# Kernel tuning notes

Measured on AMD Instinct MI355X. Metric: run time of the kernel, lower is better.

Reference implementation:

```python
import jax, jax.numpy as jnp
import numpy as np

P, F_IN, HG, C, T, E, HOUT = 4096, 64, 64, 64, 32, 65536, 12
LEAKY_SLOPE = 0.2
LN_EPS = 1e-5


def setup_inputs() -> dict:
    key = jax.random.key(0)
    ks = jax.random.split(key, 14)
    g = lambda k, shape, scale: (jax.random.normal(k, shape, jnp.float32) * scale)
    return {
        "X": jax.random.normal(ks[0], (1, P, F_IN, T), jnp.float32),
        "edge_index": jax.random.randint(ks[1], (T, 2, E), 0, P, jnp.int32),
        # GATv2 params (single head)
        "Wl": g(ks[2], (F_IN, HG), 0.1),
        "Wr": g(ks[3], (F_IN, HG), 0.1),
        "att": g(ks[4], (HG,), 0.1),
        "gat_b": g(ks[5], (HG,), 0.02),
        # 1x1 time conv (HG -> C) and 1x1 residual conv (F_IN -> C)
        "W_time": g(ks[6], (C, HG), 0.1),
        "b_time": g(ks[7], (C,), 0.02),
        "W_res": g(ks[8], (C, F_IN), 0.1),
        "b_res": g(ks[9], (C,), 0.02),
        # LayerNorm over channel dim C
        "ln_g": jnp.ones((C,), jnp.float32),
        "ln_b": jnp.zeros((C,), jnp.float32),
        # final conv: Conv2d(in=T, out=HOUT, kernel=(1, C)) -> weight (HOUT, T, C)
        "W_final": g(ks[10], (HOUT, T, C), 0.05),
        "b_final": g(ks[11], (HOUT,), 0.02),
    }


def reference(X, edge_index, Wl, Wr, att, gat_b, W_time, b_time, W_res, b_res,
              ln_g, ln_b, W_final, b_final):
    Pn = X.shape[1]

    def gat_t(x, edges):
        # x: (P, F_IN), edges: (2, E) with edges[0]=src j, edges[1]=dst i
        src, dst = edges[0], edges[1]
        hl = x @ Wl                      # (P, HG) messages
        hr = x @ Wr                      # (P, HG) query side
        e = jax.nn.leaky_relu(hl[src] + hr[dst], LEAKY_SLOPE) @ att  # (E,)
        emax = jax.ops.segment_max(e, dst, num_segments=Pn)
        ex = jnp.exp(e - emax[dst])
        den = jax.ops.segment_sum(ex, dst, num_segments=Pn)
        alpha = ex / den[dst]            # softmax over in-edges of each dst
        return jax.ops.segment_sum(alpha[:, None] * hl[src], dst,
                                   num_segments=Pn) + gat_b  # (P, HG)

    xs = jnp.moveaxis(X[0], -1, 0)                     # (T, P, F_IN)
    X_hat = jax.nn.relu(jax.vmap(gat_t)(xs, edge_index))  # (T, P, HG)

    th = jnp.einsum('tph,ch->tpc', X_hat, W_time) + b_time  # time conv 1x1
    rs = jnp.einsum('tpf,cf->tpc', xs, W_res) + b_res       # residual conv 1x1
    y = jax.nn.relu(th + rs)                                 # (T, P, C)

    mu = jnp.mean(y, axis=-1, keepdims=True)
    var = jnp.var(y, axis=-1, keepdims=True)
    yn = (y - mu) * jax.lax.rsqrt(var + LN_EPS) * ln_g + ln_b  # (T, P, C)

    # final conv: in-channels = T, kernel (1, C) -> contract over t and c
    out = jnp.einsum('tpc,otc->po', yn, W_final) + b_final     # (P, HOUT)
    return out[None]                                           # (1, P, HOUT)
```

## Files before the change

### kernel.cpp

```cpp
#include <hip/hip_runtime.h>
#include <math.h>

#define NP 4096
#define F_IN 64
#define HG 64
#define NC 64
#define NT 32
#define NE 65536
#define HOUT 12
#define LEAKY 0.2f
#define LN_EPS 1e-5f

template <int CTRL>
__device__ __forceinline__ float dppadd(float v, float x) {
    int r = __builtin_amdgcn_update_dpp(0, __builtin_bit_cast(int, x), CTRL, 0xF, 0xF, false);
    return v + __builtin_bit_cast(float, r);
}
__device__ __forceinline__ float rowsum16(float v) {
    v = dppadd<0x128>(v, v);
    v = dppadd<0x124>(v, v);
    v = dppadd<0x122>(v, v);
    v = dppadd<0x121>(v, v);
    return v;
}
__device__ __forceinline__ float xrowsum(float v) {
    v = dppadd<0x142>(v, v);
    v = dppadd<0x143>(v, v);
    return v;
}
__device__ __forceinline__ float rdlane(float v, int l) {
    return __builtin_bit_cast(float, __builtin_amdgcn_readlane(__builtin_bit_cast(int, v), l));
}
__device__ __forceinline__ float wavered63(float v) {
    v = rowsum16(v);
    v = xrowsum(v);
    return rdlane(v, 63);
}
__device__ __forceinline__ float laneXorSum(float v) {
    v += __shfl_xor(v, 16, 64);
    v += __shfl_xor(v, 32, 64);
    return v;
}
__device__ __forceinline__ int waveSumInt(int v) {
#pragma unroll
    for (int d = 1; d < 64; d <<= 1) v += __shfl_xor(v, d, 64);
    return v;
}

#define FMA4(Acomp, B, r)                                                     \
    acc[r][0] += (Acomp) * (B).x; acc[r][1] += (Acomp) * (B).y;               \
    acc[r][2] += (Acomp) * (B).z; acc[r][3] += (Acomp) * (B).w;

__global__ __launch_bounds__(256) void k_prep(const float* __restrict__ W_time,
        const float* __restrict__ W_res,
        float* __restrict__ wtT, float* __restrict__ wrT) {
    int b = blockIdx.x, tid = threadIdx.x;
    if (b < 16) {
        int i = b * 256 + tid;
        wtT[i] = W_time[(i & 63) * 64 + (i >> 6)];
    } else {
        int i = (b - 16) * 256 + tid;
        wrT[i] = W_res[(i & 63) * 64 + (i >> 6)];
    }
}

__global__ __launch_bounds__(256) void k_hlhr(const float* __restrict__ X,
        const float* __restrict__ Wl, const float* __restrict__ Wr,
        const float* __restrict__ wrT, const float* __restrict__ b_res,
        float* __restrict__ hl, float* __restrict__ hr, float* __restrict__ rs) {
    __shared__ float xs[2][F_IN][36];
    __shared__ float bk[F_IN][132];
    int p0 = blockIdx.x * 2, tid = threadIdx.x;
    const float4* Xp = (const float4*)(X + (size_t)p0 * F_IN * NT);
    for (int i4 = tid; i4 < 1024; i4 += 256) {
        int pp = i4 >> 9, f = (i4 >> 3) & 63, t0 = (i4 & 7) * 4;
        *(float4*)&xs[pp][f][t0] = Xp[i4];
    }
    for (int i = tid; i < F_IN * HG; i += 256) {
        int f = i >> 6, h = i & 63;
        bk[f][h] = Wl[i];
        bk[f][64 + h] = Wr[i];
    }
    __syncthreads();
    {
        int ng = tid & 31, tg = tid >> 5;
        int n0 = ng * 4, col = (ng & 15) * 4, t0 = tg * 4;
        float acc[8][4];
#pragma unroll
        for (int i = 0; i < 8; ++i)
#pragma unroll
            for (int j = 0; j < 4; ++j) acc[i][j] = 0.f;
#pragma unroll 4
        for (int f = 0; f < F_IN; ++f) {
            float4 B = *(const float4*)&bk[f][n0];
            float4 A0 = *(const float4*)&xs[0][f][t0];
            float4 A1 = *(const float4*)&xs[1][f][t0];
            FMA4(A0.x, B, 0) FMA4(A0.y, B, 1) FMA4(A0.z, B, 2) FMA4(A0.w, B, 3)
            FMA4(A1.x, B, 4) FMA4(A1.y, B, 5) FMA4(A1.z, B, 6) FMA4(A1.w, B, 7)
        }
#pragma unroll
        for (int pp = 0; pp < 2; ++pp) {
#pragma unroll
            for (int i = 0; i < 4; ++i) {
                size_t rb = ((size_t)(t0 + i) * NP + p0 + pp) * HG;
                float4 v;
                v.x = acc[pp * 4 + i][0]; v.y = acc[pp * 4 + i][1];
                v.z = acc[pp * 4 + i][2]; v.w = acc[pp * 4 + i][3];
                if (ng < 16) *(float4*)&hl[rb + col] = v;
                else         *(float4*)&hr[rb + col] = v;
            }
        }
    }
    __syncthreads();
    for (int i = tid; i < F_IN * NC; i += 256) bk[i >> 6][i & 63] = wrT[i];
    __syncthreads();
    {
        int cg = tid & 15, tg = tid >> 4;
        int c0 = cg * 4, t0 = tg * 2;
        float4 br4 = *(const float4*)&b_res[c0];
        float acc[4][4];
#pragma unroll
        for (int i = 0; i < 4; ++i) {
            acc[i][0] = br4.x; acc[i][1] = br4.y; acc[i][2] = br4.z; acc[i][3] = br4.w;
        }
#pragma unroll 4
        for (int f = 0; f < F_IN; ++f) {
            float4 B = *(const float4*)&bk[f][c0];
            float2 A0 = *(const float2*)&xs[0][f][t0];
            float2 A1 = *(const float2*)&xs[1][f][t0];
            FMA4(A0.x, B, 0) FMA4(A0.y, B, 1)
            FMA4(A1.x, B, 2) FMA4(A1.y, B, 3)
        }
#pragma unroll
        for (int pp = 0; pp < 2; ++pp) {
#pragma unroll
            for (int i = 0; i < 2; ++i) {
                float4 v;
                v.x = acc[pp * 2 + i][0]; v.y = acc[pp * 2 + i][1];
                v.z = acc[pp * 2 + i][2]; v.w = acc[pp * 2 + i][3];
                *(float4*)&rs[((size_t)(t0 + i) * NP + p0 + pp) * NC + c0] = v;
            }
        }
    }
}

__global__ __launch_bounds__(256) void k_count(const int* __restrict__ EI,
        int* __restrict__ cnt2, int* __restrict__ segsum2) {
    __shared__ int loc[1024];
    int b = blockIdx.x;
    int j = b >> 3;
    int t = (b & 7) + 8 * (j & 3);
    int cr = j >> 2;
    int c = cr & 3, r = cr >> 2;
    int tid = threadIdx.x;
    loc[tid] = 0; loc[tid + 256] = 0; loc[tid + 512] = 0; loc[tid + 768] = 0;
    __syncthreads();
    int base = r << 10;
    const int4* dstA = (const int4*)(EI + (size_t)t * 2 * NE + NE) + c * (NE / 16);
    for (int i = tid; i < NE / 16; i += 256) {
        int4 d = dstA[i];
        if ((d.x >> 10) == r) atomicAdd(&loc[d.x - base], 1);
        if ((d.y >> 10) == r) atomicAdd(&loc[d.y - base], 1);
        if ((d.z >> 10) == r) atomicAdd(&loc[d.z - base], 1);
        if ((d.w >> 10) == r) atomicAdd(&loc[d.w - base], 1);
    }
    __syncthreads();
    int o = (t * 4 + c) * NP + base + tid;
    cnt2[o] = loc[tid];
    cnt2[o + 256] = loc[tid + 256];
    cnt2[o + 512] = loc[tid + 512];
    cnt2[o + 768] = loc[tid + 768];
    int wv = tid >> 6, lane = tid & 63;
    int s = loc[wv * 256 + lane] + loc[wv * 256 + lane + 64]
          + loc[wv * 256 + lane + 128] + loc[wv * 256 + lane + 192];
    s = waveSumInt(s);
    if (lane == 0) segsum2[(t * 4 + c) * 16 + r * 4 + wv] = s;
}

__global__ __launch_bounds__(256) void k_scan(const int* __restrict__ cnt2,
        const int* __restrict__ segsum2, int* __restrict__ cnt,
        int* __restrict__ start, int* __restrict__ start2) {
    __shared__ int sc[256];
    __shared__ int preS;
    int b = blockIdx.x;
    int t = b >> 4, seg = b & 15;
    int tid = threadIdx.x;
    if (tid < 64) {
        int c = tid >> 4, s = tid & 15;
        int v = (s < seg) ? segsum2[(t * 4 + c) * 16 + s] : 0;
        v = waveSumInt(v);
        if (tid == 0) preS = v;
    }
    int d = seg * 256 + tid;
    int q0 = cnt2[(t * 4 + 0) * NP + d];
    int q1 = cnt2[(t * 4 + 1) * NP + d];
    int q2 = cnt2[(t * 4 + 2) * NP + d];
    int q3 = cnt2[(t * 4 + 3) * NP + d];
    int deg = q0 + q1 + q2 + q3;
    sc[tid] = deg;
    __syncthreads();
    int pre = preS;
    for (int dd = 1; dd < 256; dd <<= 1) {
        int v = (tid >= dd) ? sc[tid - dd] : 0;
        __syncthreads();
        sc[tid] += v;
        __syncthreads();
    }
    int exc = sc[tid] - deg;
    int st = t * NE + pre + exc;
    cnt[t * NP + d] = deg;
    start[t * NP + d] = st;
    start2[(t * 4 + 0) * NP + d] = st; st += q0;
    start2[(t * 4 + 1) * NP + d] = st; st += q1;
    start2[(t * 4 + 2) * NP + d] = st; st += q2;
    start2[(t * 4 + 3) * NP + d] = st;
}

__global__ __launch_bounds__(256) void k_fill(const int* __restrict__ EI,
        const int* __restrict__ start2, int* __restrict__ ssrc) {
    __shared__ int curs_l[1024];
    int b = blockIdx.x;
    int j = b >> 3;
    int t = (b & 7) + 8 * (j & 3);
    int cr = j >> 2;
    int c = cr & 3, r = cr >> 2;
    int tid = threadIdx.x;
    int base = r << 10;
    int o = (t * 4 + c) * NP + base + tid;
    curs_l[tid] = start2[o];
    curs_l[tid + 256] = start2[o + 256];
    curs_l[tid + 512] = start2[o + 512];
    curs_l[tid + 768] = start2[o + 768];
    __syncthreads();
    const int4* srcA = (const int4*)(EI + (size_t)t * 2 * NE) + c * (NE / 16);
    const int4* dstA = (const int4*)(EI + (size_t)t * 2 * NE + NE) + c * (NE / 16);
    for (int i = tid; i < NE / 16; i += 256) {
        int4 s = srcA[i];
        int4 d = dstA[i];
        if ((d.x >> 10) == r) { int sl = atomicAdd(&curs_l[d.x - base], 1); ssrc[sl] = s.x; }
        if ((d.y >> 10) == r) { int sl = atomicAdd(&curs_l[d.y - base], 1); ssrc[sl] = s.y; }
        if ((d.z >> 10) == r) { int sl = atomicAdd(&curs_l[d.z - base], 1); ssrc[sl] = s.z; }
        if ((d.w >> 10) == r) { int sl = atomicAdd(&curs_l[d.w - base], 1); ssrc[sl] = s.w; }
    }
}

__global__ __launch_bounds__(256) void k_gat(const float* __restrict__ hl,
        float* __restrict__ hr,
        const int* __restrict__ start, const int* __restrict__ cnt,
        const int* __restrict__ ssrc,
        const float* __restrict__ att, const float* __restrict__ gat_b) {
    __shared__ int sidx[4][64];
    int b = blockIdx.x;
    int k = b >> 3;
    int t = (b & 7) + 8 * (k >> 10);
    int ws = threadIdx.x >> 6;
    int i = (k & 1023) * 4 + ws;
    int lane = threadIdx.x & 63;
    int row = lane >> 4;
    int c0 = (lane & 15) * 4;
    size_t nbase = ((size_t)t * NP + i) * HG;
    const float* hlt = hl + (size_t)t * NP * HG;
    float4 r4 = *(const float4*)&hr[nbase + c0];
    float4 at4 = *(const float4*)&att[c0];
    int s0 = start[t * NP + i];
    int deg = cnt[t * NP + i];
    float l = 0.f;
    float4 acc = {0.f, 0.f, 0.f, 0.f};
    for (int base = 0; base < deg; base += 64) {
        int chunk = deg - base;
        chunk = (chunk < 64) ? chunk : 64;
        int stage = (lane < chunk) ? lane : 0;
        sidx[ws][lane] = ssrc[s0 + base + stage];
        int nfull = chunk & ~7;
        int j = 0;
        for (; j < nfull; j += 8) {
            int src0 = sidx[ws][j + row];
            int src1 = sidx[ws][j + 4 + row];
            float4 h0 = *(const float4*)&hlt[((size_t)src0 << 6) + c0];
            float4 h1 = *(const float4*)&hlt[((size_t)src1 << 6) + c0];
            float4 z0, z1;
            z0.x = h0.x + r4.x; z0.y = h0.y + r4.y; z0.z = h0.z + r4.z; z0.w = h0.w + r4.w;
            z1.x = h1.x + r4.x; z1.y = h1.y + r4.y; z1.z = h1.z + r4.z; z1.w = h1.w + r4.w;
            z0.x = fmaxf(z0.x, LEAKY * z0.x); z0.y = fmaxf(z0.y, LEAKY * z0.y);
            z0.z = fmaxf(z0.z, LEAKY * z0.z); z0.w = fmaxf(z0.w, LEAKY * z0.w);
            z1.x = fmaxf(z1.x, LEAKY * z1.x); z1.y = fmaxf(z1.y, LEAKY * z1.y);
            z1.z = fmaxf(z1.z, LEAKY * z1.z); z1.w = fmaxf(z1.w, LEAKY * z1.w);
            float e0 = rowsum16(z0.x * at4.x + z0.y * at4.y + z0.z * at4.z + z0.w * at4.w);
            float e1 = rowsum16(z1.x * at4.x + z1.y * at4.y + z1.z * at4.z + z1.w * at4.w);
            float w0 = __expf(e0);
            float w1 = __expf(e1);
            l += w0 + w1;
            acc.x += w0 * h0.x + w1 * h1.x;
            acc.y += w0 * h0.y + w1 * h1.y;
            acc.z += w0 * h0.z + w1 * h1.z;
            acc.w += w0 * h0.w + w1 * h1.w;
        }
        for (; j < chunk; j += 4) {
            int jj = j + row;
            int src = sidx[ws][(jj < chunk) ? jj : 0];
            float4 ha = *(const float4*)&hlt[((size_t)src << 6) + c0];
            float4 za;
            za.x = ha.x + r4.x; za.y = ha.y + r4.y; za.z = ha.z + r4.z; za.w = ha.w + r4.w;
            za.x = fmaxf(za.x, LEAKY * za.x);
            za.y = fmaxf(za.y, LEAKY * za.y);
            za.z = fmaxf(za.z, LEAKY * za.z);
            za.w = fmaxf(za.w, LEAKY * za.w);
            float ep = za.x * at4.x + za.y * at4.y + za.z * at4.z + za.w * at4.w;
            float e = rowsum16(ep);
            float w = __expf(e);
            w = (jj < chunk) ? w : 0.f;
            l += w;
            acc.x += w * ha.x; acc.y += w * ha.y; acc.z += w * ha.z; acc.w += w * ha.w;
        }
    }
    float lt = laneXorSum(l);
    acc.x = laneXorSum(acc.x);
    acc.y = laneXorSum(acc.y);
    acc.z = laneXorSum(acc.z);
    acc.w = laneXorSum(acc.w);
    if (row == 0) {
        float inv = (deg > 0) ? (1.0f / lt) : 0.f;
        float4 gb = *(const float4*)&gat_b[c0];
        float4 o;
        o.x = fmaxf(acc.x * inv + gb.x, 0.f);
        o.y = fmaxf(acc.y * inv + gb.y, 0.f);
        o.z = fmaxf(acc.z * inv + gb.z, 0.f);
        o.w = fmaxf(acc.w * inv + gb.w, 0.f);
        *(float4*)&hr[nbase + c0] = o;
    }
}

__global__ __launch_bounds__(256) void k_post(const float* __restrict__ Xhat,
        const float* __restrict__ wtT, const float* __restrict__ b_time,
        const float* __restrict__ rs, const float* __restrict__ ln_g,
        const float* __restrict__ ln_b, float* __restrict__ yn) {
    __shared__ float in_t[64][68];
    __shared__ float bk[64][68];
    int bx = blockIdx.x;
    int j = bx >> 3;
    int t = (bx & 7) + 8 * (j & 3);
    int p0 = (j >> 2) * 64;
    int tid = threadIdx.x;
    const float4* src = (const float4*)(Xhat + ((size_t)t * NP + p0) * HG);
    for (int i4 = tid; i4 < 1024; i4 += 256) {
        int pp = i4 >> 4, c4 = (i4 & 15) * 4;
        *(float4*)&in_t[pp][c4] = src[i4];
    }
    const float4* wsrc = (const float4*)wtT;
    for (int i4 = tid; i4 < 1024; i4 += 256) {
        int h = i4 >> 4, c4 = (i4 & 15) * 4;
        *(float4*)&bk[h][c4] = wsrc[i4];
    }
    __syncthreads();
    int cg = tid & 15, pg = tid >> 4;
    int c0 = cg * 4, pl = pg * 4;
    float4 bt4 = *(const float4*)&b_time[c0];
    float acc[4][4];
#pragma unroll
    for (int i = 0; i < 4; ++i) {
        acc[i][0] = bt4.x; acc[i][1] = bt4.y; acc[i][2] = bt4.z; acc[i][3] = bt4.w;
    }
#pragma unroll
    for (int k4 = 0; k4 < 16; ++k4) {
        float4 A0 = *(const float4*)&in_t[pl + 0][k4 * 4];
        float4 A1 = *(const float4*)&in_t[pl + 1][k4 * 4];
        float4 A2 = *(const float4*)&in_t[pl + 2][k4 * 4];
        float4 A3 = *(const float4*)&in_t[pl + 3][k4 * 4];
        float4 B0 = *(const float4*)&bk[k4 * 4 + 0][c0];
        FMA4(A0.x, B0, 0) FMA4(A1.x, B0, 1) FMA4(A2.x, B0, 2) FMA4(A3.x, B0, 3)
        float4 B1 = *(const float4*)&bk[k4 * 4 + 1][c0];
        FMA4(A0.y, B1, 0) FMA4(A1.y, B1, 1) FMA4(A2.y, B1, 2) FMA4(A3.y, B1, 3)
        float4 B2 = *(const float4*)&bk[k4 * 4 + 2][c0];
        FMA4(A0.z, B2, 0) FMA4(A1.z, B2, 1) FMA4(A2.z, B2, 2) FMA4(A3.z, B2, 3)
        float4 B3 = *(const float4*)&bk[k4 * 4 + 3][c0];
        FMA4(A0.w, B3, 0) FMA4(A1.w, B3, 1) FMA4(A2.w, B3, 2) FMA4(A3.w, B3, 3)
    }
    float4 lg = *(const float4*)&ln_g[c0];
    float4 lb = *(const float4*)&ln_b[c0];
#pragma unroll
    for (int i = 0; i < 4; ++i) {
        size_t prow = (size_t)t * NP + p0 + pl + i;
        float4 r4 = *(const float4*)&rs[prow * NC + c0];
        float y0 = fmaxf(acc[i][0] + r4.x, 0.f), y1 = fmaxf(acc[i][1] + r4.y, 0.f);
        float y2 = fmaxf(acc[i][2] + r4.z, 0.f), y3 = fmaxf(acc[i][3] + r4.w, 0.f);
        float s = rowsum16(y0 + y1 + y2 + y3);
        float ss = rowsum16(y0 * y0 + y1 * y1 + y2 * y2 + y3 * y3);
        float mu = s * (1.f / 64.f);
        float var = ss * (1.f / 64.f) - mu * mu;
        float rsd = rsqrtf(var + LN_EPS);
        float4 o;
        o.x = (y0 - mu) * rsd * lg.x + lb.x;
        o.y = (y1 - mu) * rsd * lg.y + lb.y;
        o.z = (y2 - mu) * rsd * lg.z + lb.z;
        o.w = (y3 - mu) * rsd * lg.w + lb.w;
        *(float4*)&yn[prow * NC + c0] = o;
    }
}

__global__ __launch_bounds__(256) void k_final(const float* __restrict__ yn,
        const float* __restrict__ Wf, const float* __restrict__ bf,
        float* __restrict__ out) {
    int p = blockIdx.x * 4 + (threadIdx.x >> 6);
    int lane = threadIdx.x & 63;
    float acc[HOUT];
#pragma unroll
    for (int o = 0; o < HOUT; ++o) acc[o] = 0.f;
    for (int k = 0; k < NT; ++k) {
        float yv = yn[((size_t)k * NP + p) * NC + lane];
#pragma unroll
        for (int o = 0; o < HOUT; ++o)
            acc[o] += yv * Wf[(size_t)o * NT * NC + k * NC + lane];
    }
#pragma unroll
    for (int o = 0; o < HOUT; ++o) {
        float s = wavered63(acc[o]);
        if (lane == 0) out[p * HOUT + o] = s + bf[o];
    }
}

extern "C" void kernel_launch(void* const* d_in, const int* in_sizes, int n_in,
                              void* d_out, int out_size, void* d_ws, size_t ws_size,
                              hipStream_t stream) {
    const float* X      = (const float*)d_in[0];
    const int*   EI     = (const int*)d_in[1];
    const float* Wl     = (const float*)d_in[2];
    const float* Wr     = (const float*)d_in[3];
    const float* att    = (const float*)d_in[4];
    const float* gat_b  = (const float*)d_in[5];
    const float* W_time = (const float*)d_in[6];
    const float* b_time = (const float*)d_in[7];
    const float* W_res  = (const float*)d_in[8];
    const float* b_res  = (const float*)d_in[9];
    const float* ln_g   = (const float*)d_in[10];
    const float* ln_b   = (const float*)d_in[11];
    const float* Wf     = (const float*)d_in[12];
    const float* bf     = (const float*)d_in[13];
    float* out = (float*)d_out;

    char* ws = (char*)d_ws;
    const size_t MB = 1024 * 1024;
    float* hl    = (float*)(ws);
    float* hr    = (float*)(ws + 32 * MB);
    float* rs    = (float*)(ws + 64 * MB);
    int*   ssrc  = (int*)  (ws + 96 * MB);
    int*   cnt   = (int*)  (ws + 104 * MB);
    int*   strt  = (int*)  (ws + 104 * MB + 512 * 1024);
    float* wtT   = (float*)(ws + 105 * MB);
    float* wrT   = (float*)(ws + 105 * MB + 16384);
    int*   segs2 = (int*)  (ws + 105 * MB + 32768);
    int*   cnt2  = (int*)  (ws + 106 * MB);
    int*   strt2 = (int*)  (ws + 108 * MB);
    float* yn    = hl;

    k_prep <<<32, 256, 0, stream>>>(W_time, W_res, wtT, wrT);
    k_hlhr <<<NP / 2, 256, 0, stream>>>(X, Wl, Wr, wrT, b_res, hl, hr, rs);
    k_count<<<512, 256, 0, stream>>>(EI, cnt2, segs2);
    k_scan <<<NT * 16, 256, 0, stream>>>(cnt2, segs2, cnt, strt, strt2);
    k_fill <<<512, 256, 0, stream>>>(EI, strt2, ssrc);
    k_gat  <<<(NT * NP) / 4, 256, 0, stream>>>(hl, hr, strt, cnt, ssrc, att, gat_b);
    k_post <<<NT * (NP / 64), 256, 0, stream>>>(hr, wtT, b_time, rs, ln_g, ln_b, yn);
    k_final<<<NP / 4, 256, 0, stream>>>(yn, Wf, bf, out);
}
```

Before: 284.0 us.

## Fuse post-processing with final conv and accumulate output via atomics

Merges the time conv, residual add, LayerNorm, and final T×C contraction into one kernel. Each block handles 64 nodes over 4 time steps, accumulates partial outputs in registers, and atomically adds them into an output that k_prep pre-fills with the bias. This removes the write and re-read of the full yn intermediate (T·P·C floats) and one launch. The cost is fewer blocks (512), serialized time steps per block and atomic contention on the output. It also vectorizes weight loads into shared memory in k_hlhr.

```diff
diff --git a/kernel.cpp b/kernel.cpp
--- a/kernel.cpp
+++ b/kernel.cpp
@@ -23,19 +23,6 @@
     v = dppadd<0x121>(v, v);
     return v;
 }
-__device__ __forceinline__ float xrowsum(float v) {
-    v = dppadd<0x142>(v, v);
-    v = dppadd<0x143>(v, v);
-    return v;
-}
-__device__ __forceinline__ float rdlane(float v, int l) {
-    return __builtin_bit_cast(float, __builtin_amdgcn_readlane(__builtin_bit_cast(int, v), l));
-}
-__device__ __forceinline__ float wavered63(float v) {
-    v = rowsum16(v);
-    v = xrowsum(v);
-    return rdlane(v, 63);
-}
 __device__ __forceinline__ float laneXorSum(float v) {
     v += __shfl_xor(v, 16, 64);
     v += __shfl_xor(v, 32, 64);
@@ -52,15 +39,18 @@
     acc[r][2] += (Acomp) * (B).z; acc[r][3] += (Acomp) * (B).w;
 
 __global__ __launch_bounds__(256) void k_prep(const float* __restrict__ W_time,
-        const float* __restrict__ W_res,
-        float* __restrict__ wtT, float* __restrict__ wrT) {
+        const float* __restrict__ W_res, const float* __restrict__ bf,
+        float* __restrict__ wtT, float* __restrict__ wrT, float* __restrict__ out) {
     int b = blockIdx.x, tid = threadIdx.x;
     if (b < 16) {
         int i = b * 256 + tid;
         wtT[i] = W_time[(i & 63) * 64 + (i >> 6)];
-    } else {
+    } else if (b < 32) {
         int i = (b - 16) * 256 + tid;
         wrT[i] = W_res[(i & 63) * 64 + (i >> 6)];
+    } else {
+        int i = (b - 32) * 256 + tid;
+        out[i] = bf[i % HOUT];
     }
 }
 
@@ -76,10 +66,12 @@
         int pp = i4 >> 9, f = (i4 >> 3) & 63, t0 = (i4 & 7) * 4;
         *(float4*)&xs[pp][f][t0] = Xp[i4];
     }
-    for (int i = tid; i < F_IN * HG; i += 256) {
-        int f = i >> 6, h = i & 63;
-        bk[f][h] = Wl[i];
-        bk[f][64 + h] = Wr[i];
+    const float4* Wl4 = (const float4*)Wl;
+    const float4* Wr4 = (const float4*)Wr;
+    for (int i4 = tid; i4 < 1024; i4 += 256) {
+        int f = i4 >> 4, h4 = (i4 & 15) * 4;
+        *(float4*)&bk[f][h4] = Wl4[i4];
+        *(float4*)&bk[f][64 + h4] = Wr4[i4];
     }
     __syncthreads();
     {
@@ -112,7 +104,13 @@
         }
     }
     __syncthreads();
-    for (int i = tid; i < F_IN * NC; i += 256) bk[i >> 6][i & 63] = wrT[i];
+    {
+        const float4* wrT4 = (const float4*)wrT;
+        for (int i4 = tid; i4 < 1024; i4 += 256) {
+            int f = i4 >> 4, c4 = (i4 & 15) * 4;
+            *(float4*)&bk[f][c4] = wrT4[i4];
+        }
+    }
     __syncthreads();
     {
         int cg = tid & 15, tg = tid >> 4;
@@ -330,91 +328,99 @@
     }
 }
 
-__global__ __launch_bounds__(256) void k_post(const float* __restrict__ Xhat,
+__global__ __launch_bounds__(256) void k_pf(const float* __restrict__ Xhat,
         const float* __restrict__ wtT, const float* __restrict__ b_time,
         const float* __restrict__ rs, const float* __restrict__ ln_g,
-        const float* __restrict__ ln_b, float* __restrict__ yn) {
+        const float* __restrict__ ln_b, const float* __restrict__ Wf,
+        float* __restrict__ out) {
     __shared__ float in_t[64][68];
     __shared__ float bk[64][68];
     int bx = blockIdx.x;
-    int j = bx >> 3;
-    int t = (bx & 7) + 8 * (j & 3);
-    int p0 = (j >> 2) * 64;
+    int tc = bx & 7;
+    int p0 = (bx >> 3) * 64;
     int tid = threadIdx.x;
-    const float4* src = (const float4*)(Xhat + ((size_t)t * NP + p0) * HG);
-    for (int i4 = tid; i4 < 1024; i4 += 256) {
-        int pp = i4 >> 4, c4 = (i4 & 15) * 4;
-        *(float4*)&in_t[pp][c4] = src[i4];
-    }
     const float4* wsrc = (const float4*)wtT;
     for (int i4 = tid; i4 < 1024; i4 += 256) {
         int h = i4 >> 4, c4 = (i4 & 15) * 4;
         *(float4*)&bk[h][c4] = wsrc[i4];
     }
-    __syncthreads();
     int cg = tid & 15, pg = tid >> 4;
     int c0 = cg * 4, pl = pg * 4;
     float4 bt4 = *(const float4*)&b_time[c0];
-    float acc[4][4];
-#pragma unroll
-    for (int i = 0; i < 4; ++i) {
-        acc[i][0] = bt4.x; acc[i][1] = bt4.y; acc[i][2] = bt4.z; acc[i][3] = bt4.w;
-    }
-#pragma unroll
-    for (int k4 = 0; k4 < 16; ++k4) {
-        float4 A0 = *(const float4*)&in_t[pl + 0][k4 * 4];
-        float4 A1 = *(const float4*)&in_t[pl + 1][k4 * 4];
-        float4 A2 = *(const float4*)&in_t[pl + 2][k4 * 4];
-        float4 A3 = *(const float4*)&in_t[pl + 3][k4 * 4];
-        float4 B0 = *(const float4*)&bk[k4 * 4 + 0][c0];
-        FMA4(A0.x, B0, 0) FMA4(A1.x, B0, 1) FMA4(A2.x, B0, 2) FMA4(A3.x, B0, 3)
-        float4 B1 = *(const float4*)&bk[k4 * 4 + 1][c0];
-        FMA4(A0.y, B1, 0) FMA4(A1.y, B1, 1) FMA4(A2.y, B1, 2) FMA4(A3.y, B1, 3)
-        float4 B2 = *(const float4*)&bk[k4 * 4 + 2][c0];
-        FMA4(A0.z, B2, 0) FMA4(A1.z, B2, 1) FMA4(A2.z, B2, 2) FMA4(A3.z, B2, 3)
-        float4 B3 = *(const float4*)&bk[k4 * 4 + 3][c0];
-        FMA4(A0.w, B3, 0) FMA4(A1.w, B3, 1) FMA4(A2.w, B3, 2) FMA4(A3.w, B3, 3)
-    }
     float4 lg = *(const float4*)&ln_g[c0];
     float4 lb = *(const float4*)&ln_b[c0];
-#pragma unroll
-    for (int i = 0; i < 4; ++i) {
-        size_t prow = (size_t)t * NP + p0 + pl + i;
-        float4 r4 = *(const float4*)&rs[prow * NC + c0];
-        float y0 = fmaxf(acc[i][0] + r4.x, 0.f), y1 = fmaxf(acc[i][1] + r4.y, 0.f);
-        float y2 = fmaxf(acc[i][2] + r4.z, 0.f), y3 = fmaxf(acc[i][3] + r4.w, 0.f);
-        float s = rowsum16(y0 + y1 + y2 + y3);
-        float ss = rowsum16(y0 * y0 + y1 * y1 + y2 * y2 + y3 * y3);
-        float mu = s * (1.f / 64.f);
-        float var = ss * (1.f / 64.f) - mu * mu;
-        float rsd = rsqrtf(var + LN_EPS);
-        float4 o;
-        o.x = (y0 - mu) * rsd * lg.x + lb.x;
-        o.y = (y1 - mu) * rsd * lg.y + lb.y;
-        o.z = (y2 - mu) * rsd * lg.z + lb.z;
-        o.w = (y3 - mu) * rsd * lg.w + lb.w;
-        *(float4*)&yn[prow * NC + c0] = o;
-    }
-}
-
-__global__ __launch_bounds__(256) void k_final(const float* __restrict__ yn,
-        const float* __restrict__ Wf, const float* __restrict__ bf,
-        float* __restrict__ out) {
-    int p = blockIdx.x * 4 + (threadIdx.x >> 6);
-    int lane = threadIdx.x & 63;
-    float acc[HOUT];
-#pragma unroll
-    for (int o = 0; o < HOUT; ++o) acc[o] = 0.f;
-    for (int k = 0; k < NT; ++k) {
-        float yv = yn[((size_t)k * NP + p) * NC + lane];
-#pragma unroll
-        for (int o = 0; o < HOUT; ++o)
-            acc[o] += yv * Wf[(size_t)o * NT * NC + k * NC + lane];
-    }
-#pragma unroll
-    for (int o = 0; o < HOUT; ++o) {
-        float s = wavered63(acc[o]);
-        if (lane == 0) out[p * HOUT + o] = s + bf[o];
+    float ot[4][HOUT];
+#pragma unroll
+    for (int i = 0; i < 4; ++i)
+#pragma unroll
+        for (int o = 0; o < HOUT; ++o) ot[i][o] = 0.f;
+    for (int ti = 0; ti < 4; ++ti) {
+        int t = tc + ti * 8;
+        __syncthreads();
+        const float4* src = (const float4*)(Xhat + ((size_t)t * NP + p0) * HG);
+        for (int i4 = tid; i4 < 1024; i4 += 256) {
+            int pp = i4 >> 4, c4 = (i4 & 15) * 4;
+            *(float4*)&in_t[pp][c4] = src[i4];
+        }
+        __syncthreads();
+        float acc[4][4];
+#pragma unroll
+        for (int i = 0; i < 4; ++i) {
+            acc[i][0] = bt4.x; acc[i][1] = bt4.y; acc[i][2] = bt4.z; acc[i][3] = bt4.w;
+        }
+#pragma unroll
+        for (int k4 = 0; k4 < 16; ++k4) {
+            float4 A0 = *(const float4*)&in_t[pl + 0][k4 * 4];
+            float4 A1 = *(const float4*)&in_t[pl + 1][k4 * 4];
+            float4 A2 = *(const float4*)&in_t[pl + 2][k4 * 4];
+            float4 A3 = *(const float4*)&in_t[pl + 3][k4 * 4];
+            float4 B0 = *(const float4*)&bk[k4 * 4 + 0][c0];
+            FMA4(A0.x, B0, 0) FMA4(A1.x, B0, 1) FMA4(A2.x, B0, 2) FMA4(A3.x, B0, 3)
+            float4 B1 = *(const float4*)&bk[k4 * 4 + 1][c0];
+            FMA4(A0.y, B1, 0) FMA4(A1.y, B1, 1) FMA4(A2.y, B1, 2) FMA4(A3.y, B1, 3)
+            float4 B2 = *(const float4*)&bk[k4 * 4 + 2][c0];
+            FMA4(A0.z, B2, 0) FMA4(A1.z, B2, 1) FMA4(A2.z, B2, 2) FMA4(A3.z, B2, 3)
+            float4 B3 = *(const float4*)&bk[k4 * 4 + 3][c0];
+            FMA4(A0.w, B3, 0) FMA4(A1.w, B3, 1) FMA4(A2.w, B3, 2) FMA4(A3.w, B3, 3)
+        }
+        float4 ynv[4];
+#pragma unroll
+        for (int i = 0; i < 4; ++i) {
+            size_t prow = (size_t)t * NP + p0 + pl + i;
+            float4 r4 = *(const float4*)&rs[prow * NC + c0];
+            float y0 = fmaxf(acc[i][0] + r4.x, 0.f), y1 = fmaxf(acc[i][1] + r4.y, 0.f);
+            float y2 = fmaxf(acc[i][2] + r4.z, 0.f), y3 = fmaxf(acc[i][3] + r4.w, 0.f);
+            float s = rowsum16(y0 + y1 + y2 + y3);
+            float ss = rowsum16(y0 * y0 + y1 * y1 + y2 * y2 + y3 * y3);
+            float mu = s * (1.f / 64.f);
+            float var = ss * (1.f / 64.f) - mu * mu;
+            float rsd = rsqrtf(var + LN_EPS);
+            ynv[i].x = (y0 - mu) * rsd * lg.x + lb.x;
+            ynv[i].y = (y1 - mu) * rsd * lg.y + lb.y;
+            ynv[i].z = (y2 - mu) * rsd * lg.z + lb.z;
+            ynv[i].w = (y3 - mu) * rsd * lg.w + lb.w;
+        }
+#pragma unroll
+        for (int o = 0; o < HOUT; ++o) {
+            float4 w4 = *(const float4*)&Wf[(size_t)o * NT * NC + t * NC + c0];
+#pragma unroll
+            for (int i = 0; i < 4; ++i)
+                ot[i][o] += ynv[i].x * w4.x + ynv[i].y * w4.y
+                          + ynv[i].z * w4.z + ynv[i].w * w4.w;
+        }
+    }
+#pragma unroll
+    for (int i = 0; i < 4; ++i)
+#pragma unroll
+        for (int o = 0; o < HOUT; ++o) ot[i][o] = rowsum16(ot[i][o]);
+    if (cg == 0) {
+#pragma unroll
+        for (int i = 0; i < 4; ++i) {
+            int p = p0 + pl + i;
+#pragma unroll
+            for (int o = 0; o < HOUT; ++o)
+                atomicAdd(&out[p * HOUT + o], ot[i][o]);
+        }
     }
 }
 
@@ -450,14 +456,12 @@
     int*   segs2 = (int*)  (ws + 105 * MB + 32768);
     int*   cnt2  = (int*)  (ws + 106 * MB);
     int*   strt2 = (int*)  (ws + 108 * MB);
-    float* yn    = hl;
-
-    k_prep <<<32, 256, 0, stream>>>(W_time, W_res, wtT, wrT);
+
+    k_prep <<<224, 256, 0, stream>>>(W_time, W_res, bf, wtT, wrT, out);
     k_hlhr <<<NP / 2, 256, 0, stream>>>(X, Wl, Wr, wrT, b_res, hl, hr, rs);
     k_count<<<512, 256, 0, stream>>>(EI, cnt2, segs2);
     k_scan <<<NT * 16, 256, 0, stream>>>(cnt2, segs2, cnt, strt, strt2);
     k_fill <<<512, 256, 0, stream>>>(EI, strt2, ssrc);
     k_gat  <<<(NT * NP) / 4, 256, 0, stream>>>(hl, hr, strt, cnt, ssrc, att, gat_b);
-    k_post <<<NT * (NP / 64), 256, 0, stream>>>(hr, wtT, b_time, rs, ln_g, ln_b, yn);
-    k_final<<<NP / 4, 256, 0, stream>>>(yn, Wf, bf, out);
-}
+    k_pf   <<<512, 256, 0, stream>>>(hr, wtT, b_time, rs, ln_g, ln_b, Wf, out);
+}
```

After: 286.3 us. No clear change (+0.8%).
